# Kernel optimization log

Measured on AMD Instinct MI355X. Metric: run time of the kernel, lower is better.

The kernel has to match this reference:

```python
import jax, jax.numpy as jnp
import numpy as np

EPS = 1e-10
SHIFT = 1  # surface_thickness
WHITE_BG = True


def setup_inputs() -> dict:
    key = jax.random.key(0)
    k1, k2, k3 = jax.random.split(key, 3)
    B, R, N, F = 8, 16384, 128, 3
    rays_densities = jax.random.uniform(k1, (B, R, N, 1), dtype=jnp.float32)
    rays_features = jax.random.uniform(k2, (B, R, N, F), dtype=jnp.float32)
    # monotone-ish depths along ray (values only need to be floats; sort for realism)
    lengths = jnp.sort(jax.random.uniform(k3, (B, R, N), dtype=jnp.float32), axis=-1)
    return {"rays_densities": rays_densities, "rays_features": rays_features, "lengths": lengths}


def reference(rays_densities, rays_features, lengths):
    d = rays_densities[..., 0]                       # (B, R, N)
    cp = jnp.cumprod(1.0 + EPS - d, axis=-1)         # absorption cumprod
    absorption = jnp.concatenate(
        [jnp.ones_like(cp[..., :SHIFT]), cp[..., :-SHIFT]], axis=-1
    )                                                # shifted cumprod
    weights = d * absorption                         # (B, R, N)
    features = jnp.einsum('brn,brnf->brf', weights, rays_features)  # (B, R, F)
    depths = jnp.sum(weights * lengths, axis=-1, keepdims=True)     # (B, R, 1)
    pix_alpha = jnp.sum(weights, axis=-1)                            # (B, R)
    if WHITE_BG:
        features = features + 1.0 - pix_alpha[..., None]
    depths = depths + (1.0 - pix_alpha[..., None]) * lengths[..., -1:]
    return jnp.concatenate([features, depths], axis=-1)             # (B, R, F+1)
```

## Files before the change

kernel.cpp:

```cpp
#include <hip/hip_runtime.h>

#define RM_EPS 1e-10f
#define RM_N   128
#define RM_F   3

__global__ __launch_bounds__(256) void raymarch_kernel(
    const float* __restrict__ dens,
    const float* __restrict__ feat,
    const float* __restrict__ len,
    float* __restrict__ out,
    int n_rays)
{
    const int wave = (int)((blockIdx.x * blockDim.x + threadIdx.x) >> 6);
    const int lane = (int)(threadIdx.x & 63);
    if (wave >= n_rays) return;
    const long long ray = wave;

    const float2 d2 = ((const float2*)(dens + ray * RM_N))[lane];
    const float2 l2 = ((const float2*)(len  + ray * RM_N))[lane];
    const float2* fp = (const float2*)(feat + ray * (RM_N * RM_F)) + lane * 3;
    const float2 fa = fp[0];
    const float2 fb = fp[1];
    const float2 fc = fp[2];

    const float t0 = 1.0f + RM_EPS - d2.x;
    const float t1 = 1.0f + RM_EPS - d2.y;

    float p = t0 * t1;
    #pragma unroll
    for (int off = 1; off < 64; off <<= 1) {
        float q = __shfl_up(p, off);
        p *= (lane >= off) ? q : 1.0f;
    }
    float e = __shfl_up(p, 1);
    if (lane == 0) e = 1.0f;

    const float w0 = d2.x * e;
    const float w1 = d2.y * e * t0;

    float s0 = w0 * fa.x + w1 * fb.y;
    float s1 = w0 * fa.y + w1 * fc.x;
    float s2 = w0 * fb.x + w1 * fc.y;
    float sd = w0 * l2.x + w1 * l2.y;
    float sa = w0 + w1;

    #pragma unroll
    for (int off = 32; off > 0; off >>= 1) {
        s0 += __shfl_xor(s0, off);
        s1 += __shfl_xor(s1, off);
        s2 += __shfl_xor(s2, off);
        sd += __shfl_xor(sd, off);
        sa += __shfl_xor(sa, off);
    }
    const float last_len = __shfl(l2.y, 63);

    if (lane == 0) {
        const float bg = 1.0f - sa;
        float4 o;
        o.x = s0 + bg;
        o.y = s1 + bg;
        o.z = s2 + bg;
        o.w = sd + bg * last_len;
        ((float4*)out)[ray] = o;
    }
}

extern "C" void kernel_launch(void* const* d_in, const int* in_sizes, int n_in,
                              void* d_out, int out_size, void* d_ws, size_t ws_size,
                              hipStream_t stream) {
    const float* dens = (const float*)d_in[0];
    const float* feat = (const float*)d_in[1];
    const float* len  = (const float*)d_in[2];
    float* out = (float*)d_out;

    const int n_rays = in_sizes[0] / RM_N;
    const int waves_per_block = 256 / 64;
    const int grid = (n_rays + waves_per_block - 1) / waves_per_block;
    raymarch_kernel<<<grid, 256, 0, stream>>>(dens, feat, len, out, n_rays);
}
```

Baseline: 349.1 us.

## Process four rays per wave with sixteen lanes per ray and float4 loads

Remaps work so each 64-lane wave handles four rays, with each 16-lane segment covering one ray and each lane handling eight consecutive samples. Each lane does a local sequential cumprod and weighted accumulation, followed by a 4-step segmented shuffle scan and reduction instead of 6-step full-wave ones. Loads widen from float2 to float4, which aims to cut shuffle overhead and per-byte instruction count. More registers are used per thread.

New measurement: 349.7 us. Within noise of the previous version (+0.2%).

```diff
diff --git a/kernel.cpp b/kernel.cpp
--- a/kernel.cpp
+++ b/kernel.cpp
@@ -1,8 +1,6 @@
 #include <hip/hip_runtime.h>
 
 #define RM_EPS 1e-10f
-#define RM_N   128
-#define RM_F   3
 
 __global__ __launch_bounds__(256) void raymarch_kernel(
     const float* __restrict__ dens,
@@ -11,50 +9,64 @@
     float* __restrict__ out,
     int n_rays)
 {
-    const int wave = (int)((blockIdx.x * blockDim.x + threadIdx.x) >> 6);
-    const int lane = (int)(threadIdx.x & 63);
-    if (wave >= n_rays) return;
-    const long long ray = wave;
+    const int lane  = (int)(threadIdx.x & 63);
+    const int gwave = (int)((blockIdx.x * blockDim.x + threadIdx.x) >> 6);
+    const int rseg  = lane >> 4;
+    const int sl    = lane & 15;
+    const long long ray = (long long)gwave * 4 + rseg;
+    if (ray >= n_rays) return;
 
-    const float2 d2 = ((const float2*)(dens + ray * RM_N))[lane];
-    const float2 l2 = ((const float2*)(len  + ray * RM_N))[lane];
-    const float2* fp = (const float2*)(feat + ray * (RM_N * RM_F)) + lane * 3;
-    const float2 fa = fp[0];
-    const float2 fb = fp[1];
-    const float2 fc = fp[2];
+    const float4* dp = (const float4*)(dens + ray * 128 + sl * 8);
+    const float4* lp = (const float4*)(len  + ray * 128 + sl * 8);
+    const float4* fp = (const float4*)(feat + ray * 384 + sl * 24);
+    const float4 d0 = dp[0], d1 = dp[1];
+    const float4 l0 = lp[0], l1 = lp[1];
+    const float4 f0 = fp[0], f1 = fp[1], f2 = fp[2];
+    const float4 f3 = fp[3], f4 = fp[4], f5 = fp[5];
 
-    const float t0 = 1.0f + RM_EPS - d2.x;
-    const float t1 = 1.0f + RM_EPS - d2.y;
+    const float d[8]  = {d0.x,d0.y,d0.z,d0.w, d1.x,d1.y,d1.z,d1.w};
+    const float ll[8] = {l0.x,l0.y,l0.z,l0.w, l1.x,l1.y,l1.z,l1.w};
+    const float f[24] = {f0.x,f0.y,f0.z,f0.w, f1.x,f1.y,f1.z,f1.w,
+                         f2.x,f2.y,f2.z,f2.w, f3.x,f3.y,f3.z,f3.w,
+                         f4.x,f4.y,f4.z,f4.w, f5.x,f5.y,f5.z,f5.w};
 
-    float p = t0 * t1;
+    float cp = 1.0f;
     #pragma unroll
-    for (int off = 1; off < 64; off <<= 1) {
-        float q = __shfl_up(p, off);
-        p *= (lane >= off) ? q : 1.0f;
+    for (int i = 0; i < 8; ++i) cp *= (1.0f + RM_EPS - d[i]);
+
+    float p = cp;
+    #pragma unroll
+    for (int off = 1; off < 16; off <<= 1) {
+        float q = __shfl_up(p, off, 16);
+        if (sl >= off) p *= q;
     }
-    float e = __shfl_up(p, 1);
-    if (lane == 0) e = 1.0f;
+    float e = __shfl_up(p, 1, 16);
+    if (sl == 0) e = 1.0f;
 
-    const float w0 = d2.x * e;
-    const float w1 = d2.y * e * t0;
-
-    float s0 = w0 * fa.x + w1 * fb.y;
-    float s1 = w0 * fa.y + w1 * fc.x;
-    float s2 = w0 * fb.x + w1 * fc.y;
-    float sd = w0 * l2.x + w1 * l2.y;
-    float sa = w0 + w1;
+    float s0 = 0.f, s1 = 0.f, s2 = 0.f, sd = 0.f, sa = 0.f;
+    float run = e;
+    #pragma unroll
+    for (int i = 0; i < 8; ++i) {
+        const float wi = d[i] * run;
+        s0 += wi * f[3*i+0];
+        s1 += wi * f[3*i+1];
+        s2 += wi * f[3*i+2];
+        sd += wi * ll[i];
+        sa += wi;
+        run *= (1.0f + RM_EPS - d[i]);
+    }
 
     #pragma unroll
-    for (int off = 32; off > 0; off >>= 1) {
-        s0 += __shfl_xor(s0, off);
-        s1 += __shfl_xor(s1, off);
-        s2 += __shfl_xor(s2, off);
-        sd += __shfl_xor(sd, off);
-        sa += __shfl_xor(sa, off);
+    for (int off = 8; off > 0; off >>= 1) {
+        s0 += __shfl_xor(s0, off, 16);
+        s1 += __shfl_xor(s1, off, 16);
+        s2 += __shfl_xor(s2, off, 16);
+        sd += __shfl_xor(sd, off, 16);
+        sa += __shfl_xor(sa, off, 16);
     }
-    const float last_len = __shfl(l2.y, 63);
+    const float last_len = __shfl(l1.w, 15, 16);
 
-    if (lane == 0) {
+    if (sl == 0) {
         const float bg = 1.0f - sa;
         float4 o;
         o.x = s0 + bg;
@@ -73,8 +85,10 @@
     const float* len  = (const float*)d_in[2];
     float* out = (float*)d_out;
 
-    const int n_rays = in_sizes[0] / RM_N;
-    const int waves_per_block = 256 / 64;
-    const int grid = (n_rays + waves_per_block - 1) / waves_per_block;
-    raymarch_kernel<<<grid, 256, 0, stream>>>(dens, feat, len, out, n_rays);
+    const int n_rays = in_sizes[0] / 128;
+    const long long waves = (n_rays + 3) / 4;
+    const long long threads = waves * 64;
+    const int block = 256;
+    const int grid = (int)((threads + block - 1) / block);
+    raymarch_kernel<<<grid, block, 0, stream>>>(dens, feat, len, out, n_rays);
 }
```
